# Optimization experiments

Hardware: AMD Instinct MI355X
Metric: run time of the kernel (lower is better)

## Reference

```python
import jax, jax.numpy as jnp
import numpy as np

N_CLASSES = 19


def setup_inputs() -> dict:
    key = jax.random.key(0)
    k1, k2 = jax.random.split(key)
    embedding = jax.random.normal(k1, (4, 32, 128, 128), dtype=jnp.float32)
    label = jax.random.randint(k2, (4, 512, 512), 0, N_CLASSES, dtype=jnp.int64)
    return {"embedding": embedding, "label": label}


def _discriminative_loss(embedding, label, n_classes=N_CLASSES):
    N, H, W = label.shape
    C = embedding.shape[1]
    # bilinear upsample embedding to label resolution (F.upsample mode='bilinear')
    emb = jax.image.resize(embedding, (N, C, H, W), method="bilinear")
    HW = H * W
    emb = emb.reshape(N, C, HW).transpose(0, 2, 1)          # (N, HW, C)
    lab = label.reshape(N, HW)                               # (N, HW)

    onehot = jax.nn.one_hot(lab, n_classes, dtype=emb.dtype)  # (N, HW, K)
    count = onehot.sum(1)                                    # (N, K)
    mask = (count > 0).astype(emb.dtype)                     # (N, K)

    # per-class embedding sum and (biased, /(count+1)) mean
    cls_sum = jnp.einsum("npc,npk->nkc", emb, onehot)       # (N, K, C)
    cls_mean = cls_sum / (count[:, :, None] + 1.0)           # (N, K, C)

    # intra-class: per-pixel squared distance to own-class mean, mean over C
    mean_pp = jnp.take_along_axis(cls_mean, lab[:, :, None], axis=1)  # (N, HW, C)
    d2 = jnp.mean((emb - mean_pp) ** 2, axis=-1)             # (N, HW)
    intra_per_cls = jnp.einsum("np,npk->nk", d2, onehot) / (count + 1.0)  # (N, K)
    n_fg = mask[:, 1:].sum(1)                                # (N,)
    l2_intra = (intra_per_cls[:, 1:] * mask[:, 1:]).sum(1) / n_fg  # (N,)

    # inter-class: pairwise mean squared distance between class means
    diff = cls_mean[:, :, None, :] - cls_mean[:, None, :, :]  # (N, K, K, C)
    inter = jnp.mean(diff ** 2, axis=-1)                     # (N, K, K)
    inter = inter * mask[:, None, :] * mask[:, :, None]
    l2_inter = inter[:, 1:, 1:].reshape(N, -1).sum(1) / (n_fg * n_fg)  # (N,)

    return l2_intra - l2_inter


def reference(embedding, label):
    return _discriminative_loss(embedding, label)
```

## Files before the change

kernel.cpp:

```cpp
#include <hip/hip_runtime.h>

#define NIMG 4
#define NCLS 19
#define CCH  32
#define LH   128
#define LW   128
#define HH   512
#define WW   512
#define HWQ  (LH*LW)
#define HWP  (HH*WW)

#define TR 8
#define TC 16
#define NTILE 128
#define TCELLS 128
#define HALO_R 36
#define HALO_C 68
#define NHALO (HALO_R*HALO_C)
#define QB2 256

#define L_ET  0
#define L_A   4224
#define L_RED 6656
#define LDS_FLOATS 9088

__device__ __forceinline__ void taps(int v, int lim, int& i0, int& i1, float& f) {
    int r = v & 3;
    int b = (v >> 2) + ((r < 2) ? -1 : 0);
    f = 0.125f + 0.25f * (float)((r + 2) & 3);
    i0 = b < 0 ? 0 : b;
    i1 = (b + 1 > lim) ? lim : (b + 1);
}

__global__ __launch_bounds__(256) void k_main(const float* __restrict__ E,
        const int* __restrict__ lab, float* __restrict__ P_sum,
        float* __restrict__ P_cnt, float* __restrict__ P_S2) {
    __shared__ float lds[LDS_FLOATS];
    const int n = blockIdx.y;
    const int tid = threadIdx.x;
    const int bid = blockIdx.x;

    if (bid < NTILE) {
        const int ty = bid >> 3, tx = bid & 7;
        const int Y0 = ty * TR, X0 = tx * TC;
        for (int i = tid; i < TCELLS * NCLS; i += 256) lds[L_A + i] = 0.f;
#pragma unroll
        for (int it = 0; it < 16; it++) {
            int idx = it * 256 + tid;
            int c = idx >> 7, cell = idx & 127;
            int cy = cell >> 4, cx = cell & 15;
            float e = E[((size_t)n * CCH + c) * HWQ + (Y0 + cy) * LW + (X0 + cx)];
            lds[L_ET + cell * 33 + c] = e;
        }
        const int* ln = lab + (size_t)n * HWP;
        const int h_lo = Y0 * 4 - 2, w_lo = X0 * 4 - 2;
        int Lv[10];
#pragma unroll
        for (int it = 0; it < 10; it++) {
            int i = it * 256 + tid;
            int hr = i / HALO_C, wc = i - hr * HALO_C;
            int h = h_lo + hr, w = w_lo + wc;
            bool ok = (i < NHALO) & (h >= 0) & (h < HH) & (w >= 0) & (w < WW);
            int hc = h < 0 ? 0 : (h > HH - 1 ? HH - 1 : h);
            int wl = w < 0 ? 0 : (w > WW - 1 ? WW - 1 : w);
            int lv = ln[hc * WW + wl];
            Lv[it] = ok ? lv : -1;
        }
        __syncthreads();
#pragma unroll
        for (int it = 0; it < 10; it++) {
            if (Lv[it] < 0) continue;
            int i = it * 256 + tid;
            int hr = i / HALO_C, wc = i - hr * HALO_C;
            int h = h_lo + hr, w = w_lo + wc;
            int y0, y1, x0, x1; float fy, fx;
            taps(h, LH - 1, y0, y1, fy);
            taps(w, LW - 1, x0, x1, fx);
            int yy[2] = {y0, y1}; float wy[2] = {1.f - fy, fy};
            int xx[2] = {x0, x1}; float wx[2] = {1.f - fx, fx};
#pragma unroll
            for (int a = 0; a < 2; a++) {
#pragma unroll
                for (int b = 0; b < 2; b++) {
                    int ry = yy[a] - Y0, rx = xx[b] - X0;
                    if (ry >= 0 && ry < TR && rx >= 0 && rx < TC)
                        atomicAdd(&lds[L_A + (ry * TC + rx) * NCLS + Lv[it]], wy[a] * wx[b]);
                }
            }
        }
        __syncthreads();
        const int g = tid >> 5, c = tid & 31;
        float acc[NCLS];
#pragma unroll
        for (int k = 0; k < NCLS; k++) acc[k] = 0.f;
#pragma unroll
        for (int j = 0; j < 16; j++) {
            int cell = g * 16 + j;
            float e = lds[L_ET + cell * 33 + c];
            const float* Ar = &lds[L_A + cell * NCLS];
#pragma unroll
            for (int k = 0; k < NCLS; k++) acc[k] = fmaf(Ar[k], e, acc[k]);
        }
#pragma unroll
        for (int k = 0; k < NCLS; k++) acc[k] += __shfl_xor(acc[k], 32);
        const int wv = tid >> 6;
        if ((tid & 63) < 32) {
#pragma unroll
            for (int k = 0; k < NCLS; k++) lds[L_RED + wv * 608 + k * 32 + c] = acc[k];
        }
        __syncthreads();
        float* Ps = P_sum + (size_t)(n * NTILE + bid) * 608;
        for (int i = tid; i < 608; i += 256)
            Ps[i] = lds[L_RED + i] + lds[L_RED + 608 + i]
                  + lds[L_RED + 1216 + i] + lds[L_RED + 1824 + i];
        if (tid < NCLS) {
            float s = 0.f;
            for (int cell = 0; cell < TCELLS; cell++) s += lds[L_A + cell * NCLS + tid];
            P_cnt[((size_t)n * NCLS + tid) * NTILE + bid] = s;
        }
    } else {
        const int qb = bid - NTILE;
        const int by = qb >> 1;
        const int ch0 = (qb & 1) * 16 + (tid >> 7) * 8;
        const int bx = tid & 127;
        if (tid < NCLS) lds[tid] = 0.f;
        __syncthreads();

        const float* En = E + (size_t)n * CCH * HWQ;
        const int r0 = (by == 0) ? 0 : by - 1;
        const int r2 = (by == LH - 1) ? LH - 1 : by + 1;
        const int c0 = (bx == 0) ? 0 : bx - 1;
        const int c2 = (bx == LW - 1) ? LW - 1 : bx + 1;
        const int o0 = r0 * LW, o1 = by * LW, o2 = r2 * LW;

        float d2[16];
#pragma unroll
        for (int i = 0; i < 16; i++) d2[i] = 0.f;

#pragma unroll 2
        for (int c = 0; c < 8; c++) {
            const float* Ep = En + (size_t)(ch0 + c) * HWQ;
            float e00 = Ep[o0 + c0], e01 = Ep[o0 + bx], e02 = Ep[o0 + c2];
            float e10 = Ep[o1 + c0], e11 = Ep[o1 + bx], e12 = Ep[o1 + c2];
            float e20 = Ep[o2 + c0], e21 = Ep[o2 + bx], e22 = Ep[o2 + c2];
            float dy0 = e10 - e00, dy1 = e11 - e01, dy2 = e12 - e02;
            float dz0 = e20 - e10, dz1 = e21 - e11, dz2 = e22 - e12;
            float ry[4][3];
            ry[0][0] = fmaf(0.625f, dy0, e00); ry[0][1] = fmaf(0.625f, dy1, e01); ry[0][2] = fmaf(0.625f, dy2, e02);
            ry[1][0] = fmaf(0.875f, dy0, e00); ry[1][1] = fmaf(0.875f, dy1, e01); ry[1][2] = fmaf(0.875f, dy2, e02);
            ry[2][0] = fmaf(0.125f, dz0, e10); ry[2][1] = fmaf(0.125f, dz1, e11); ry[2][2] = fmaf(0.125f, dz2, e12);
            ry[3][0] = fmaf(0.375f, dz0, e10); ry[3][1] = fmaf(0.375f, dz1, e11); ry[3][2] = fmaf(0.375f, dz2, e12);
#pragma unroll
            for (int r = 0; r < 4; r++) {
                float da = ry[r][1] - ry[r][0], db = ry[r][2] - ry[r][1];
                float v0 = fmaf(0.625f, da, ry[r][0]);
                float v1 = fmaf(0.875f, da, ry[r][0]);
                float v2 = fmaf(0.125f, db, ry[r][1]);
                float v3 = fmaf(0.375f, db, ry[r][1]);
                d2[r * 4 + 0] = fmaf(v0, v0, d2[r * 4 + 0]);
                d2[r * 4 + 1] = fmaf(v1, v1, d2[r * 4 + 1]);
                d2[r * 4 + 2] = fmaf(v2, v2, d2[r * 4 + 2]);
                d2[r * 4 + 3] = fmaf(v3, v3, d2[r * 4 + 3]);
            }
        }
        const int* lp = lab + (size_t)n * HWP + (by * 4) * WW + bx * 4;
#pragma unroll
        for (int r = 0; r < 4; r++) {
            int4 l4 = *(const int4*)(lp + r * WW);
            atomicAdd(&lds[l4.x], d2[r * 4 + 0]);
            atomicAdd(&lds[l4.y], d2[r * 4 + 1]);
            atomicAdd(&lds[l4.z], d2[r * 4 + 2]);
            atomicAdd(&lds[l4.w], d2[r * 4 + 3]);
        }
        __syncthreads();
        if (tid < NCLS)
            P_S2[((size_t)n * NCLS + tid) * QB2 + qb] = lds[tid];
    }
}

__global__ __launch_bounds__(640) void k_final(const float* __restrict__ P_sum,
        const float* __restrict__ P_cnt, const float* __restrict__ P_S2,
        float* __restrict__ out) {
    const int n = blockIdx.x, t = threadIdx.x;
    __shared__ float csum[NCLS * 33];
    __shared__ float m[NCLS * 33];
    __shared__ float cnt[NCLS];
    __shared__ float S2[NCLS];
    __shared__ float sIntra, sNfg, sInter;
    if (t == 0) sInter = 0.f;

    if (t < NCLS * CCH) {
        const int k = t >> 5, c = t & 31;
        const float* p = P_sum + (size_t)n * NTILE * (NCLS * CCH) + t;
        float s = 0.f;
        for (int b = 0; b < NTILE; b++) s += p[b * (NCLS * CCH)];
        csum[k * 33 + c] = s;
        const float* pc = P_cnt + ((size_t)n * NCLS + k) * NTILE;
        float sc = 0.f;
        for (int i = c; i < NTILE; i += 32) sc += pc[i];
        const float* ps = P_S2 + ((size_t)n * NCLS + k) * QB2;
        float s2 = 0.f;
        for (int i = c; i < QB2; i += 32) s2 += ps[i];
#pragma unroll
        for (int mk = 16; mk >= 1; mk >>= 1) {
            sc += __shfl_xor(sc, mk);
            s2 += __shfl_xor(s2, mk);
        }
        if (c == 0) { cnt[k] = sc; S2[k] = s2; }
    }
    __syncthreads();
    if (t < NCLS * CCH) {
        const int k = t >> 5, c = t & 31;
        m[k * 33 + c] = csum[k * 33 + c] / (cnt[k] + 1.f);
    }
    __syncthreads();

    float vi = 0.f, fg = 0.f;
    if (t >= 1 && t < NCLS && cnt[t] > 0.f) {
        fg = 1.f;
        float dot = 0.f, mm = 0.f;
#pragma unroll
        for (int c = 0; c < CCH; c++) {
            float mv = m[t * 33 + c];
            dot = fmaf(mv, csum[t * 33 + c], dot);
            mm = fmaf(mv, mv, mm);
        }
        vi = (S2[t] - 2.f * dot + cnt[t] * mm) * (1.f / 32.f) / (cnt[t] + 1.f);
    }
#pragma unroll
    for (int s_ = 32; s_ >= 1; s_ >>= 1) { vi += __shfl_xor(vi, s_); fg += __shfl_xor(fg, s_); }
    if (t == 0) { sIntra = vi; sNfg = fg; }

    float ve = 0.f;
    if (t < 324) {
        int j = 1 + t / 18, k = 1 + t % 18;
        if (cnt[j] > 0.f && cnt[k] > 0.f) {
            float s = 0.f;
#pragma unroll
            for (int c = 0; c < CCH; c++) {
                float d = m[j * 33 + c] - m[k * 33 + c];
                s = fmaf(d, d, s);
            }
            ve = s * (1.f / 32.f);
        }
    }
#pragma unroll
    for (int s_ = 32; s_ >= 1; s_ >>= 1) ve += __shfl_xor(ve, s_);
    if ((t & 63) == 0) atomicAdd(&sInter, ve);
    __syncthreads();
    if (t == 0) out[n] = sIntra / sNfg - sInter / (sNfg * sNfg);
}

extern "C" void kernel_launch(void* const* d_in, const int* in_sizes, int n_in,
                              void* d_out, int out_size, void* d_ws, size_t ws_size,
                              hipStream_t stream) {
    const float* E = (const float*)d_in[0];
    const int* lab = (const int*)d_in[1];
    float* out = (float*)d_out;

    float* ws = (float*)d_ws;
    float* P_sum = ws;
    float* P_cnt = P_sum + (size_t)NIMG * NTILE * NCLS * CCH;
    float* P_S2  = P_cnt + (size_t)NIMG * NCLS * NTILE;

    k_main <<<dim3(NTILE + QB2, NIMG), dim3(256), 0, stream>>>(E, lab, P_sum, P_cnt, P_S2);
    k_final<<<dim3(NIMG), dim3(640), 0, stream>>>(P_sum, P_cnt, P_S2, out);
}
```

Baseline: 126.7 us.

## Interleave tile and S2 blocks, keep embedding in registers, per-wave LDS accumulators

Tile blocks are now interleaved with S2 blocks (every third block id) to balance load across CUs. The tile path loads embeddings straight into registers as float4 instead of staging them in LDS. The class-weight matrix uses a padded stride of 20 so it can be read with vector LDS loads, and per-class counts are accumulated with atomics during the scatter instead of a serial 128-cell sum. The S2 path gives each wave its own accumulator to reduce LDS atomic contention, at the cost of extra atomics for the counts.

After: 144.1 us. 13.7% more time.

```diff
diff --git a/kernel.cpp b/kernel.cpp
--- a/kernel.cpp
+++ b/kernel.cpp
@@ -13,16 +13,16 @@
 #define TR 8
 #define TC 16
 #define NTILE 128
-#define TCELLS 128
 #define HALO_R 36
 #define HALO_C 68
 #define NHALO (HALO_R*HALO_C)
 #define QB2 256
-
-#define L_ET  0
-#define L_A   4224
-#define L_RED 6656
-#define LDS_FLOATS 9088
+#define ASTR 20
+
+#define L_A    0
+#define L_CNT  2560
+#define L_RED  2580
+#define LDS_FLOATS 5012
 
 __device__ __forceinline__ void taps(int v, int lim, int& i0, int& i1, float& f) {
     int r = v & 3;
@@ -40,18 +40,19 @@
     const int tid = threadIdx.x;
     const int bid = blockIdx.x;
 
-    if (bid < NTILE) {
-        const int ty = bid >> 3, tx = bid & 7;
+    if (bid % 3 == 0) {
+        const int tile = bid / 3;
+        const int ty = tile >> 3, tx = tile & 7;
         const int Y0 = ty * TR, X0 = tx * TC;
-        for (int i = tid; i < TCELLS * NCLS; i += 256) lds[L_A + i] = 0.f;
-#pragma unroll
-        for (int it = 0; it < 16; it++) {
-            int idx = it * 256 + tid;
-            int c = idx >> 7, cell = idx & 127;
-            int cy = cell >> 4, cx = cell & 15;
-            float e = E[((size_t)n * CCH + c) * HWQ + (Y0 + cy) * LW + (X0 + cx)];
-            lds[L_ET + cell * 33 + c] = e;
-        }
+        for (int i = tid; i < L_RED; i += 256) lds[i] = 0.f;
+
+        const int g = tid >> 5, c = tid & 31;
+        const float* Erow = E + ((size_t)n * CCH + c) * HWQ + (Y0 + g) * LW + X0;
+        const float4 e0 = *(const float4*)(Erow + 0);
+        const float4 e1 = *(const float4*)(Erow + 4);
+        const float4 e2 = *(const float4*)(Erow + 8);
+        const float4 e3 = *(const float4*)(Erow + 12);
+
         const int* ln = lab + (size_t)n * HWP;
         const int h_lo = Y0 * 4 - 2, w_lo = X0 * 4 - 2;
         int Lv[10];
@@ -78,28 +79,47 @@
             taps(w, LW - 1, x0, x1, fx);
             int yy[2] = {y0, y1}; float wy[2] = {1.f - fy, fy};
             int xx[2] = {x0, x1}; float wx[2] = {1.f - fx, fx};
+            float wtot = 0.f;
 #pragma unroll
             for (int a = 0; a < 2; a++) {
 #pragma unroll
                 for (int b = 0; b < 2; b++) {
                     int ry = yy[a] - Y0, rx = xx[b] - X0;
-                    if (ry >= 0 && ry < TR && rx >= 0 && rx < TC)
-                        atomicAdd(&lds[L_A + (ry * TC + rx) * NCLS + Lv[it]], wy[a] * wx[b]);
+                    if (ry >= 0 && ry < TR && rx >= 0 && rx < TC) {
+                        float w_ = wy[a] * wx[b];
+                        atomicAdd(&lds[L_A + (ry * TC + rx) * ASTR + Lv[it]], w_);
+                        wtot += w_;
+                    }
                 }
             }
-        }
-        __syncthreads();
-        const int g = tid >> 5, c = tid & 31;
+            if (wtot > 0.f) atomicAdd(&lds[L_CNT + Lv[it]], wtot);
+        }
+        __syncthreads();
+
+        float ev[16] = {e0.x, e0.y, e0.z, e0.w, e1.x, e1.y, e1.z, e1.w,
+                        e2.x, e2.y, e2.z, e2.w, e3.x, e3.y, e3.z, e3.w};
         float acc[NCLS];
 #pragma unroll
         for (int k = 0; k < NCLS; k++) acc[k] = 0.f;
 #pragma unroll
-        for (int j = 0; j < 16; j++) {
-            int cell = g * 16 + j;
-            float e = lds[L_ET + cell * 33 + c];
-            const float* Ar = &lds[L_A + cell * NCLS];
-#pragma unroll
-            for (int k = 0; k < NCLS; k++) acc[k] = fmaf(Ar[k], e, acc[k]);
+        for (int cx = 0; cx < TC; cx++) {
+            const float* Ar = &lds[L_A + (g * TC + cx) * ASTR];
+            const float4 a0 = *(const float4*)(Ar + 0);
+            const float4 a1 = *(const float4*)(Ar + 4);
+            const float4 a2 = *(const float4*)(Ar + 8);
+            const float4 a3 = *(const float4*)(Ar + 12);
+            const float a16 = Ar[16], a17 = Ar[17], a18 = Ar[18];
+            const float e = ev[cx];
+            acc[0]  = fmaf(a0.x, e, acc[0]);  acc[1]  = fmaf(a0.y, e, acc[1]);
+            acc[2]  = fmaf(a0.z, e, acc[2]);  acc[3]  = fmaf(a0.w, e, acc[3]);
+            acc[4]  = fmaf(a1.x, e, acc[4]);  acc[5]  = fmaf(a1.y, e, acc[5]);
+            acc[6]  = fmaf(a1.z, e, acc[6]);  acc[7]  = fmaf(a1.w, e, acc[7]);
+            acc[8]  = fmaf(a2.x, e, acc[8]);  acc[9]  = fmaf(a2.y, e, acc[9]);
+            acc[10] = fmaf(a2.z, e, acc[10]); acc[11] = fmaf(a2.w, e, acc[11]);
+            acc[12] = fmaf(a3.x, e, acc[12]); acc[13] = fmaf(a3.y, e, acc[13]);
+            acc[14] = fmaf(a3.z, e, acc[14]); acc[15] = fmaf(a3.w, e, acc[15]);
+            acc[16] = fmaf(a16, e, acc[16]);  acc[17] = fmaf(a17, e, acc[17]);
+            acc[18] = fmaf(a18, e, acc[18]);
         }
 #pragma unroll
         for (int k = 0; k < NCLS; k++) acc[k] += __shfl_xor(acc[k], 32);
@@ -109,21 +129,19 @@
             for (int k = 0; k < NCLS; k++) lds[L_RED + wv * 608 + k * 32 + c] = acc[k];
         }
         __syncthreads();
-        float* Ps = P_sum + (size_t)(n * NTILE + bid) * 608;
+        float* Ps = P_sum + (size_t)(n * NTILE + tile) * 608;
         for (int i = tid; i < 608; i += 256)
             Ps[i] = lds[L_RED + i] + lds[L_RED + 608 + i]
                   + lds[L_RED + 1216 + i] + lds[L_RED + 1824 + i];
-        if (tid < NCLS) {
-            float s = 0.f;
-            for (int cell = 0; cell < TCELLS; cell++) s += lds[L_A + cell * NCLS + tid];
-            P_cnt[((size_t)n * NCLS + tid) * NTILE + bid] = s;
-        }
+        if (tid < NCLS)
+            P_cnt[((size_t)n * NCLS + tid) * NTILE + tile] = lds[L_CNT + tid];
     } else {
-        const int qb = bid - NTILE;
+        const int qb = bid - bid / 3 - 1;
         const int by = qb >> 1;
         const int ch0 = (qb & 1) * 16 + (tid >> 7) * 8;
         const int bx = tid & 127;
-        if (tid < NCLS) lds[tid] = 0.f;
+        const int wv = tid >> 6;
+        if ((tid & 63) < ASTR) lds[wv * ASTR + (tid & 63)] = 0.f;
         __syncthreads();
 
         const float* En = E + (size_t)n * CCH * HWQ;
@@ -164,17 +182,19 @@
             }
         }
         const int* lp = lab + (size_t)n * HWP + (by * 4) * WW + bx * 4;
+        float* accW = &lds[wv * ASTR];
 #pragma unroll
         for (int r = 0; r < 4; r++) {
             int4 l4 = *(const int4*)(lp + r * WW);
-            atomicAdd(&lds[l4.x], d2[r * 4 + 0]);
-            atomicAdd(&lds[l4.y], d2[r * 4 + 1]);
-            atomicAdd(&lds[l4.z], d2[r * 4 + 2]);
-            atomicAdd(&lds[l4.w], d2[r * 4 + 3]);
+            atomicAdd(&accW[l4.x], d2[r * 4 + 0]);
+            atomicAdd(&accW[l4.y], d2[r * 4 + 1]);
+            atomicAdd(&accW[l4.z], d2[r * 4 + 2]);
+            atomicAdd(&accW[l4.w], d2[r * 4 + 3]);
         }
         __syncthreads();
         if (tid < NCLS)
-            P_S2[((size_t)n * NCLS + tid) * QB2 + qb] = lds[tid];
+            P_S2[((size_t)n * NCLS + tid) * QB2 + qb] =
+                lds[tid] + lds[ASTR + tid] + lds[2 * ASTR + tid] + lds[3 * ASTR + tid];
     }
 }
 
```
